# Optimization experiments

Hardware: AMD Instinct MI355X
Metric: run time of the kernel (lower is better)

## Reference

```python
import jax, jax.numpy as jnp
import numpy as np

N_HEADS = 12


def setup_inputs() -> dict:
    key = jax.random.key(0)
    ks = jax.random.split(key, 4)
    B, S, D = 2, 2048, 768
    x = jax.random.normal(ks[0], (B, S, D), dtype=jnp.float32)
    # nn.Linear-style init scale ~ 1/sqrt(D) to keep logits reasonable
    scale = 1.0 / np.sqrt(D)
    Wq = jax.random.normal(ks[1], (D, D), dtype=jnp.float32) * scale
    Wk = jax.random.normal(ks[2], (D, D), dtype=jnp.float32) * scale
    Wv = jax.random.normal(ks[3], (D, D), dtype=jnp.float32) * scale
    bq = jnp.zeros((D,), jnp.float32)
    bk = jnp.zeros((D,), jnp.float32)
    bv = jnp.zeros((D,), jnp.float32)
    mask = jnp.ones((B, S), jnp.int32)
    return {"x": x, "Wq": Wq, "bq": bq, "Wk": Wk, "bk": bk,
            "Wv": Wv, "bv": bv, "mask": mask}


def reference(x, Wq, bq, Wk, bk, Wv, bv, mask):
    B, S, D = x.shape
    H = N_HEADS
    W = D // H
    # q,k,v: (B,S,D) -> (B,H,S,W)
    def proj(Wm, bm):
        return (x @ Wm.T + bm).reshape(B, S, H, W).transpose(0, 2, 1, 3)
    q, k, v = proj(Wq, bq), proj(Wk, bk), proj(Wv, bv)
    scores = jnp.einsum("bhsw,bhtw->bhst", q, k) / jnp.sqrt(
        jnp.asarray(W, x.dtype))
    # mask: (B,S) -> broadcast over query positions; 0 -> -1e20
    scores = jnp.where(mask[:, None, None, :] == 0,
                       jnp.asarray(-1e20, scores.dtype), scores)
    attn = jax.nn.softmax(scores, axis=-1)  # (B,H,S,S)
    # dropout p=0.0 (eval) -> identity
    ctx = jnp.einsum("bhst,bhtw->bhsw", attn, v)
    hidden = ctx.transpose(0, 2, 1, 3).reshape(B, S, D)
    return hidden
```

## Files before the change

### kernel.cpp

```cpp
#include <hip/hip_runtime.h>
#include <hip/hip_bf16.h>
#include <stdint.h>


typedef __attribute__((ext_vector_type(8))) short bf16x8;
typedef __attribute__((ext_vector_type(4))) float f32x4;
typedef __attribute__((ext_vector_type(16))) float f32x16;
typedef __attribute__((ext_vector_type(8))) unsigned short u16x8;

#define MFMA16(a, b, c) __builtin_amdgcn_mfma_f32_16x16x32_bf16((a), (b), (c), 0, 0, 0)
#define MFMA32(a, b, c) __builtin_amdgcn_mfma_f32_32x32x16_bf16((a), (b), (c), 0, 0, 0)
#define SWZ(row, colb) ((colb) ^ (((row) & 7) << 4))

union U32x4BF {
  unsigned u[4];
  bf16x8 v;
};

__device__ __forceinline__ void gl_lds16(const void* g, void* l) {
  __builtin_amdgcn_global_load_lds(
      (__attribute__((address_space(1))) void*)const_cast<void*>(g),
      (__attribute__((address_space(3))) void*)l, 16, 0, 0);
}

__device__ __forceinline__ unsigned short f2bf(float x) {
  unsigned int v = __float_as_uint(x);
  return (unsigned short)((v + 0x7fffu + ((v >> 16) & 1u)) >> 16);
}

__global__ __launch_bounds__(256) void cvt_all(
    const float* __restrict__ x, const float* __restrict__ wq,
    const float* __restrict__ wk, const float* __restrict__ wv,
    unsigned short* __restrict__ xb, unsigned short* __restrict__ wb) {
  int i = blockIdx.x * 256 + threadIdx.x;
  const float* s;
  unsigned short* d;
  int off;
  if (i < 393216)      { s = x;  d = xb;            off = i; }
  else if (i < 466944) { s = wq; d = wb;            off = i - 393216; }
  else if (i < 540672) { s = wk; d = wb + 589824;   off = i - 466944; }
  else                 { s = wv; d = wb + 1179648;  off = i - 540672; }
  const float4* sp = (const float4*)s + (size_t)off * 2;
  float4 a = sp[0], b2 = sp[1];
  u16x8 o;
  o[0] = f2bf(a.x); o[1] = f2bf(a.y); o[2] = f2bf(a.z); o[3] = f2bf(a.w);
  o[4] = f2bf(b2.x); o[5] = f2bf(b2.y); o[6] = f2bf(b2.z); o[7] = f2bf(b2.w);
  *((u16x8*)d + off) = o;
}

__global__ __launch_bounds__(256) void proj_gemm(
    const unsigned short* __restrict__ xb, const unsigned short* __restrict__ wb,
    const float* __restrict__ bq, const float* __restrict__ bk, const float* __restrict__ bv,
    unsigned short* __restrict__ qw, unsigned short* __restrict__ kw,
    unsigned short* __restrict__ vw) {
  __shared__ __align__(16) char psmem[36864];
  const int t = threadIdx.x, lane = t & 63, w = t >> 6;
  const int lo = lane & 15, hi = lane >> 4;
  const int mbase = blockIdx.x * 64;
  const int wsel = blockIdx.y / 6;
  const int nbase = (blockIdx.y % 6) * 128;
  const char* xc = (const char*)xb;
  const char* wmc = (const char*)(wb + (size_t)wsel * 589824);

  const int tA = t * 16;
  const int arA = tA >> 7, acA = (tA & 127) ^ ((arA & 7) << 4);
  const int mA = ((acA >> 6) << 5) + arA, kA = acA & 63;
  const int pB0 = t * 16, pB1 = t * 16 + 4096;
  const int rB0 = pB0 >> 7, cB0 = (pB0 & 127) ^ ((rB0 & 7) << 4);
  const int nB0 = ((cB0 >> 6) << 6) + rB0, kB0 = cB0 & 63;
  const int rB1 = pB1 >> 7, cB1 = (pB1 & 127) ^ ((rB1 & 7) << 4);
  const int nB1 = ((cB1 >> 6) << 6) + rB1, kB1 = cB1 & 63;

  const char* xa0 = xc + (size_t)(mbase + mA) * 1536 + kA;
  const char* wa0 = wmc + (size_t)(nbase + nB0) * 1536 + kB0;
  const char* wa1 = wmc + (size_t)(nbase + nB1) * 1536 + kB1;

#define PSTAGE(BUF)                              \
  do {                                           \
    char* lb = psmem + (BUF) * 12288;            \
    gl_lds16(xa0, lb + tA);                      \
    gl_lds16(wa0, lb + 4096 + pB0);              \
    gl_lds16(wa1, lb + 4096 + pB1);              \
    xa0 += 64; wa0 += 64; wa1 += 64;             \
  } while (0)

  f32x4 acc[4][2];
#pragma unroll
  for (int i = 0; i < 4; i++)
#pragma unroll
    for (int j = 0; j < 2; j++) acc[i][j] = (f32x4){0.f, 0.f, 0.f, 0.f};

  PSTAGE(0);
  PSTAGE(1);
  int cur = 0, sb = 2;
#pragma unroll 1
  for (int it = 0; it < 24; ++it) {
    if (it < 22) {
      PSTAGE(sb);
      asm volatile("s_waitcnt vmcnt(6)" ::: "memory");
    } else if (it == 22) {
      asm volatile("s_waitcnt vmcnt(3)" ::: "memory");
    } else {
      asm volatile("s_waitcnt vmcnt(0)" ::: "memory");
    }
    __builtin_amdgcn_s_barrier();
    const char* lA = psmem + cur * 12288;
    const char* lB = lA + 4096;

    bf16x8 af[4], bf[2];
#pragma unroll
    for (int mf = 0; mf < 4; mf++) {
      int row = mf * 16 + lo;
      af[mf] = *(const bf16x8*)(lA + (row & 31) * 128 +
                                ((((row >> 5) << 6) + hi * 16) ^ ((row & 7) << 4)));
    }
#pragma unroll
    for (int nf = 0; nf < 2; nf++) {
      int n = w * 32 + nf * 16 + lo;
      bf[nf] = *(const bf16x8*)(lB + (n & 63) * 128 +
                                ((((n >> 6) << 6) + hi * 16) ^ ((n & 7) << 4)));
    }

    __builtin_amdgcn_s_setprio(1);
    if (wsel == 2) {
#pragma unroll
      for (int mf = 0; mf < 4; mf++)
#pragma unroll
        for (int nf = 0; nf < 2; nf++) acc[mf][nf] = MFMA16(bf[nf], af[mf], acc[mf][nf]);
    } else {
#pragma unroll
      for (int mf = 0; mf < 4; mf++)
#pragma unroll
        for (int nf = 0; nf < 2; nf++) acc[mf][nf] = MFMA16(af[mf], bf[nf], acc[mf][nf]);
    }
    __builtin_amdgcn_s_setprio(0);
    __builtin_amdgcn_s_barrier();
    cur = (cur == 2) ? 0 : cur + 1;
    sb = (sb == 2) ? 0 : sb + 1;
  }
#undef PSTAGE

  const float QSCALE = 0.125f * 1.44269504089f;
  if (wsel == 2) {
#pragma unroll
    for (int nf = 0; nf < 2; nf++) {
#pragma unroll
      for (int mf = 0; mf < 4; mf++) {
#pragma unroll
        for (int r = 0; r < 4; r++) {
          int n = nbase + w * 32 + nf * 16 + hi * 4 + r;
          int m = mbase + mf * 16 + lo;
          int b_ = m >> 11, s = m & 2047;
          int h = n >> 6, wcol = n & 63;
          float val = acc[mf][nf][r] + bv[n];
          vw[(((size_t)b_ * 12 + h) * 64 + wcol) * 2048 + s] = f2bf(val);
        }
      }
    }
  } else {
    const float* bias = (wsel == 0) ? bq : bk;
#pragma unroll
    for (int nf = 0; nf < 2; nf++) {
      int n = nbase + w * 32 + nf * 16 + lo;
      float bv_ = bias[n];
      int h = n >> 6, wcol = n & 63;
#pragma unroll
      for (int mf = 0; mf < 4; mf++) {
#pragma unroll
        for (int r = 0; r < 4; r++) {
          int m = mbase + mf * 16 + hi * 4 + r;
          int b_ = m >> 11, s = m & 2047;
          float val = acc[mf][nf][r] + bv_;
          size_t bhh = (size_t)b_ * 12 + h;
          if (wsel == 0)
            qw[(bhh * 2048 + s) * 64 + wcol] = f2bf(val * QSCALE);
          else
            kw[(bhh * 2048 + s) * 64 + wcol] = f2bf(val);
        }
      }
    }
  }
}

__global__ __launch_bounds__(256) void relayout_kv(
    const unsigned short* kw, const unsigned short* __restrict__ vwT,
    unsigned short* __restrict__ kx, unsigned short* vx) {
  __shared__ __align__(16) char rsm[32768];
  const int t = threadIdx.x;
  const int bid = blockIdx.x;
  const int xcd = bid & 7, sidx = bid >> 3;
  const int bh = xcd + 8 * (sidx % 3);
  const int ktq = sidx / 3;
  const size_t bhb = (size_t)bh * 262144;
  const int kt0 = ktq * 4;

  {
    const int key = t >> 3;
    const int d0 = (t & 7) * 8;
    const char* ksrc = (const char*)kw + bhb + (size_t)kt0 * 4096 + key * 128 + d0 * 2;
    char* kldst = rsm + (d0 >> 4) * 1024 + ((d0 >> 3) & 1) * 512 + key * 16;
#pragma unroll
    for (int c = 0; c < 4; c++)
      *(u16x8*)(kldst + c * 4096) = *(const u16x8*)(ksrc + c * 4096);
  }
  {
    const int w = t >> 2;
    const int sl0 = (t & 3) * 8;
    const char* vsrc = (const char*)vwT + bhb + (size_t)w * 4096 + (kt0 * 32 + sl0) * 2;
    char* vldst = rsm + 16384 + (w >> 5) * 2048 + ((sl0 >> 4) & 1) * 1024 +
                  ((sl0 >> 3) & 1) * 512 + (w & 31) * 16;
#pragma unroll
    for (int c = 0; c < 4; c++)
      *(u16x8*)(vldst + c * 4096) = *(const u16x8*)(vsrc + c * 64);
  }
  __syncthreads();

  char* kdst = (char*)kx + bhb + (size_t)ktq * 16384;
  char* vdst = (char*)vx + bhb + (size_t)ktq * 16384;
#pragma unroll
  for (int c = 0; c < 4; c++) {
    int lb = c * 4096 + t * 16;
    *(u16x8*)(kdst + lb) = *(const u16x8*)(rsm + lb);
    *(u16x8*)(vdst + lb) = *(const u16x8*)(rsm + 16384 + lb);
  }
}

__global__ __launch_bounds__(256) void attn_kernel(
    const unsigned short* __restrict__ qw, const unsigned short* __restrict__ kx,
    const unsigned short* __restrict__ vx, const int* __restrict__ mask,
    float* __restrict__ out) {
  __shared__ __align__(16) char smem[17152];
  const int t = threadIdx.x, lane = t & 63, wave = t >> 6;
  const int wq = wave >> 1, wk = wave & 1;
  const int l31 = lane & 31, hl = lane >> 5;
  const int bid = blockIdx.x;
  const int xcd = bid & 7, sidx = bid >> 3;
  const int bh = xcd + 8 * (sidx % 3);
  const int qb = sidx / 3;
  const int b = bh / 12, hh = bh - b * 12;

  {
    const int* mb = mask + (size_t)b * 2048 + t * 8;
    int4 a0 = *(const int4*)mb;
    int4 a1 = *(const int4*)(mb + 4);
    unsigned by = (unsigned)(a0.x != 0) | ((unsigned)(a0.y != 0) << 1) |
                  ((unsigned)(a0.z != 0) << 2) | ((unsigned)(a0.w != 0) << 3) |
                  ((unsigned)(a1.x != 0) << 4) | ((unsigned)(a1.y != 0) << 5) |
                  ((unsigned)(a1.z != 0) << 6) | ((unsigned)(a1.w != 0) << 7);
    smem[16384 + t] = (char)by;
  }
  __syncthreads();
  const unsigned balv = *(const unsigned*)(smem + 16384 + (wk * 32 + l31) * 4);

  bf16x8 qv[4];
  {
    int qrow = qb * 64 + wq * 32 + l31;
    const char* qp = (const char*)qw + ((size_t)bh * 2048 + qrow) * 128 + hl * 16;
#pragma unroll
    for (int s = 0; s < 4; s++) qv[s] = *(const bf16x8*)(qp + s * 32);
  }

  const char* kp = (const char*)kx + (size_t)bh * 262144 + (size_t)wk * 131072 + lane * 16;
  const char* vp = (const char*)vx + (size_t)bh * 262144 + (size_t)wk * 131072 + lane * 16;

  f32x16 oacc[2];
#pragma unroll
  for (int wh = 0; wh < 2; wh++)
#pragma unroll
    for (int g = 0; g < 16; g++) oacc[wh][g] = 0.f;
  float lacc = 0.f;

  bf16x8 ka0 = *(const bf16x8*)(kp);
  bf16x8 ka1 = *(const bf16x8*)(kp + 1024);
  bf16x8 ka2 = *(const bf16x8*)(kp + 2048);
  bf16x8 ka3 = *(const bf16x8*)(kp + 3072);
  kp += 4096;

#pragma unroll 2
  for (int it = 0; it < 32; ++it) {
    bf16x8 v00 = *(const bf16x8*)(vp);
    bf16x8 v01 = *(const bf16x8*)(vp + 1024);
    bf16x8 v10 = *(const bf16x8*)(vp + 2048);
    bf16x8 v11 = *(const bf16x8*)(vp + 3072);
    vp += 4096;

    f32x16 sc;
#pragma unroll
    for (int g = 0; g < 16; g++) sc[g] = 0.f;
    __builtin_amdgcn_s_setprio(1);
    sc = MFMA32(ka0, qv[0], sc);
    sc = MFMA32(ka1, qv[1], sc);
    sc = MFMA32(ka2, qv[2], sc);
    sc = MFMA32(ka3, qv[3], sc);
    __builtin_amdgcn_s_setprio(0);

    ka0 = *(const bf16x8*)(kp);
    ka1 = *(const bf16x8*)(kp + 1024);
    ka2 = *(const bf16x8*)(kp + 2048);
    ka3 = *(const bf16x8*)(kp + 3072);
    kp += 4096;

    unsigned bal = __builtin_amdgcn_readlane(balv, it);
    if (bal != 0xFFFFFFFFu) {
#pragma unroll
      for (int g = 0; g < 16; g++) {
        int key = (g & 3) + 8 * (g >> 2) + 4 * hl;
        if (!((bal >> key) & 1)) sc[g] = -30000.f;
      }
    }

#pragma unroll
    for (int g = 0; g < 16; g++) {
      float e_;
      asm("v_exp_f32 %0, %1" : "=v"(e_) : "v"(sc[g]));
      sc[g] = e_;
    }
    unsigned pk[4][2];
#pragma unroll
    for (int m = 0; m < 4; m++) {
      asm("v_cvt_pk_bf16_f32 %0, %1, %2" : "=v"(pk[m][0]) : "v"(sc[4 * m]), "v"(sc[4 * m + 1]));
      asm("v_cvt_pk_bf16_f32 %0, %1, %2" : "=v"(pk[m][1]) : "v"(sc[4 * m + 2]), "v"(sc[4 * m + 3]));
    }
    U32x4BF apv[2];
#pragma unroll
    for (int sp = 0; sp < 2; sp++)
#pragma unroll
      for (int cp = 0; cp < 2; cp++) {
        unsigned xx = pk[2 * sp][cp], yy = pk[2 * sp + 1][cp];
        asm("v_permlane32_swap_b32 %0, %1" : "+v"(xx), "+v"(yy));
        apv[sp].u[cp] = xx;
        apv[sp].u[2 + cp] = yy;
      }

    __builtin_amdgcn_s_setprio(1);
    oacc[0] = MFMA32(apv[0].v, v00, oacc[0]);
    oacc[0] = MFMA32(apv[1].v, v01, oacc[0]);
    oacc[1] = MFMA32(apv[0].v, v10, oacc[1]);
    oacc[1] = MFMA32(apv[1].v, v11, oacc[1]);
    __builtin_amdgcn_s_setprio(0);

    lacc += (((sc[0] + sc[1]) + (sc[2] + sc[3])) + ((sc[4] + sc[5]) + (sc[6] + sc[7]))) +
            (((sc[8] + sc[9]) + (sc[10] + sc[11])) + ((sc[12] + sc[13]) + (sc[14] + sc[15])));
  }

  lacc += __shfl_xor(lacc, 32);
  if (lane < 32)
    *(float*)(smem + 16640 + (((wq * 32 + l31) << 1) + wk) * 4) = lacc;
  if (wk == 1) {
#pragma unroll
    for (int wh = 0; wh < 2; wh++) {
      int vrow = wh * 32 + l31;
#pragma unroll
      for (int m = 0; m < 4; m++) {
        f32x4 part = (f32x4){oacc[wh][4 * m], oacc[wh][4 * m + 1],
                             oacc[wh][4 * m + 2], oacc[wh][4 * m + 3]};
        *(f32x4*)(smem + wq * 8192 + vrow * 128 + SWZ(vrow, hl * 16 + m * 32)) = part;
      }
    }
  }
  __syncthreads();
  if (wk == 0) {
    float linv[16];
#pragma unroll
    for (int g = 0; g < 16; g++) {
      int qrow = 4 * hl + (g & 3) + 8 * (g >> 2);
      float2 lp = *(const float2*)(smem + 16640 + ((wq * 32 + qrow) << 3));
      linv[g] = __builtin_amdgcn_rcpf(lp.x + lp.y);
    }
#pragma unroll
    for (int wh = 0; wh < 2; wh++) {
      int vrow = wh * 32 + l31;
#pragma unroll
      for (int m = 0; m < 4; m++) {
        f32x4 part = *(const f32x4*)(smem + wq * 8192 + vrow * 128 + SWZ(vrow, hl * 16 + m * 32));
#pragma unroll
        for (int r = 0; r < 4; r++) {
          int g = 4 * m + r;
          int qrow = 4 * hl + r + 8 * m;
          float val = (oacc[wh][g] + part[r]) * linv[g];
          out[((size_t)b * 2048 + qb * 64 + wq * 32 + qrow) * 768 + hh * 64 + wh * 32 + l31] =
              val;
        }
      }
    }
  }
}

extern "C" void kernel_launch(void* const* d_in, const int* in_sizes, int n_in,
                              void* d_out, int out_size, void* d_ws, size_t ws_size,
                              hipStream_t stream) {
  (void)in_sizes; (void)n_in; (void)out_size; (void)ws_size;
  const float* x  = (const float*)d_in[0];
  const float* Wq = (const float*)d_in[1];
  const float* bq = (const float*)d_in[2];
  const float* Wk = (const float*)d_in[3];
  const float* bk = (const float*)d_in[4];
  const float* Wv = (const float*)d_in[5];
  const float* bv = (const float*)d_in[6];
  const int* mask = (const int*)d_in[7];
  float* out = (float*)d_out;

  char* ws = (char*)d_ws;
  unsigned short* xb  = (unsigned short*)(ws);
  unsigned short* wb  = (unsigned short*)(ws + 6291456);
  unsigned short* qw  = (unsigned short*)(ws + 9830400);
  unsigned short* kw  = (unsigned short*)(ws + 16121856);
  unsigned short* vwT = (unsigned short*)(ws + 22413312);
  unsigned short* kx  = (unsigned short*)(ws);
  unsigned short* vx  = (unsigned short*)(ws + 16121856);

  cvt_all<<<2400, 256, 0, stream>>>(x, Wq, Wk, Wv, xb, wb);
  proj_gemm<<<dim3(64, 18), 256, 0, stream>>>(xb, wb, bq, bk, bv, qw, kw, vwT);
  relayout_kv<<<384, 256, 0, stream>>>(kw, vwT, kx, vx);
  attn_kernel<<<768, 256, 0, stream>>>(qw, kx, vx, mask, out);
}
```

Before: 83.21 us.

## Software-pipeline QK^T MFMA one tile ahead of softmax and PV

Restructures the attention inner loop so the score MFMAs for tile i are issued while tile i-1's mask, exp, bf16 packing and PV MFMAs are processed, ping-ponging between two score accumulators. This is meant to hide MFMA latency and keep the matrix units busy during the VALU exp/convert work. It costs an extra 16-float accumulator in registers, which may lower occupancy, and adds a prologue and epilogue.

```diff
diff --git a/kernel.cpp b/kernel.cpp
--- a/kernel.cpp
+++ b/kernel.cpp
@@ -263,85 +263,110 @@
   const char* kp = (const char*)kx + (size_t)bh * 262144 + (size_t)wk * 131072 + lane * 16;
   const char* vp = (const char*)vx + (size_t)bh * 262144 + (size_t)wk * 131072 + lane * 16;
 
-  f32x16 oacc[2];
+  f32x16 oacc[2], scA, scB;
 #pragma unroll
   for (int wh = 0; wh < 2; wh++)
 #pragma unroll
     for (int g = 0; g < 16; g++) oacc[wh][g] = 0.f;
   float lacc = 0.f;
-
-  bf16x8 ka0 = *(const bf16x8*)(kp);
-  bf16x8 ka1 = *(const bf16x8*)(kp + 1024);
-  bf16x8 ka2 = *(const bf16x8*)(kp + 2048);
-  bf16x8 ka3 = *(const bf16x8*)(kp + 3072);
+  bf16x8 v00, v01, v10, v11;
+  bf16x8 ka0, ka1, ka2, ka3;
+
+#define SMPV(J_, SCP_)                                                                   \
+  {                                                                                      \
+    unsigned bal_ = __builtin_amdgcn_readlane(balv, (J_));                               \
+    if (bal_ != 0xFFFFFFFFu) {                                                           \
+      _Pragma("unroll") for (int g = 0; g < 16; g++) {                                   \
+        int key_ = (g & 3) + 8 * (g >> 2) + 4 * hl;                                      \
+        if (!((bal_ >> key_) & 1)) SCP_[g] = -30000.f;                                   \
+      }                                                                                  \
+    }                                                                                    \
+    _Pragma("unroll") for (int g = 0; g < 16; g++) {                                     \
+      float e_;                                                                          \
+      asm("v_exp_f32 %0, %1" : "=v"(e_) : "v"(SCP_[g]));                                 \
+      SCP_[g] = e_;                                                                      \
+    }                                                                                    \
+    unsigned pk_[4][2];                                                                  \
+    _Pragma("unroll") for (int m = 0; m < 4; m++) {                                      \
+      asm("v_cvt_pk_bf16_f32 %0, %1, %2"                                                 \
+          : "=v"(pk_[m][0]) : "v"(SCP_[4 * m]), "v"(SCP_[4 * m + 1]));                   \
+      asm("v_cvt_pk_bf16_f32 %0, %1, %2"                                                 \
+          : "=v"(pk_[m][1]) : "v"(SCP_[4 * m + 2]), "v"(SCP_[4 * m + 3]));               \
+    }                                                                                    \
+    U32x4BF apv_[2];                                                                     \
+    _Pragma("unroll") for (int sp = 0; sp < 2; sp++)                                     \
+        _Pragma("unroll") for (int cp = 0; cp < 2; cp++) {                               \
+      unsigned xx_ = pk_[2 * sp][cp], yy_ = pk_[2 * sp + 1][cp];                         \
+      asm("v_permlane32_swap_b32 %0, %1" : "+v"(xx_), "+v"(yy_));                        \
+      apv_[sp].u[cp] = xx_;                                                              \
+      apv_[sp].u[2 + cp] = yy_;                                                          \
+    }                                                                                    \
+    __builtin_amdgcn_s_setprio(1);                                                       \
+    oacc[0] = MFMA32(apv_[0].v, v00, oacc[0]);                                           \
+    oacc[0] = MFMA32(apv_[1].v, v01, oacc[0]);                                           \
+    oacc[1] = MFMA32(apv_[0].v, v10, oacc[1]);                                           \
+    oacc[1] = MFMA32(apv_[1].v, v11, oacc[1]);                                           \
+    __builtin_amdgcn_s_setprio(0);                                                       \
+    lacc += (((SCP_[0] + SCP_[1]) + (SCP_[2] + SCP_[3])) +                               \
+             ((SCP_[4] + SCP_[5]) + (SCP_[6] + SCP_[7]))) +                              \
+            (((SCP_[8] + SCP_[9]) + (SCP_[10] + SCP_[11])) +                             \
+             ((SCP_[12] + SCP_[13]) + (SCP_[14] + SCP_[15])));                           \
+  }
+
+#define BODY(IT_, SCQ_, SCP_)                                                            \
+  {                                                                                      \
+    v00 = *(const bf16x8*)(vp);                                                          \
+    v01 = *(const bf16x8*)(vp + 1024);                                                   \
+    v10 = *(const bf16x8*)(vp + 2048);                                                   \
+    v11 = *(const bf16x8*)(vp + 3072);                                                   \
+    vp += 4096;                                                                          \
+    _Pragma("unroll") for (int g = 0; g < 16; g++) SCQ_[g] = 0.f;                        \
+    __builtin_amdgcn_s_setprio(1);                                                       \
+    SCQ_ = MFMA32(ka0, qv[0], SCQ_);                                                     \
+    SCQ_ = MFMA32(ka1, qv[1], SCQ_);                                                     \
+    SCQ_ = MFMA32(ka2, qv[2], SCQ_);                                                     \
+    SCQ_ = MFMA32(ka3, qv[3], SCQ_);                                                     \
+    __builtin_amdgcn_s_setprio(0);                                                       \
+    ka0 = *(const bf16x8*)(kp);                                                          \
+    ka1 = *(const bf16x8*)(kp + 1024);                                                   \
+    ka2 = *(const bf16x8*)(kp + 2048);                                                   \
+    ka3 = *(const bf16x8*)(kp + 3072);                                                   \
+    kp += 4096;                                                                          \
+    SMPV((IT_) - 1, SCP_);                                                               \
+  }
+
+  ka0 = *(const bf16x8*)(kp);
+  ka1 = *(const bf16x8*)(kp + 1024);
+  ka2 = *(const bf16x8*)(kp + 2048);
+  ka3 = *(const bf16x8*)(kp + 3072);
   kp += 4096;
-
-#pragma unroll 2
-  for (int it = 0; it < 32; ++it) {
-    bf16x8 v00 = *(const bf16x8*)(vp);
-    bf16x8 v01 = *(const bf16x8*)(vp + 1024);
-    bf16x8 v10 = *(const bf16x8*)(vp + 2048);
-    bf16x8 v11 = *(const bf16x8*)(vp + 3072);
-    vp += 4096;
-
-    f32x16 sc;
-#pragma unroll
-    for (int g = 0; g < 16; g++) sc[g] = 0.f;
-    __builtin_amdgcn_s_setprio(1);
-    sc = MFMA32(ka0, qv[0], sc);
-    sc = MFMA32(ka1, qv[1], sc);
-    sc = MFMA32(ka2, qv[2], sc);
-    sc = MFMA32(ka3, qv[3], sc);
-    __builtin_amdgcn_s_setprio(0);
-
-    ka0 = *(const bf16x8*)(kp);
-    ka1 = *(const bf16x8*)(kp + 1024);
-    ka2 = *(const bf16x8*)(kp + 2048);
-    ka3 = *(const bf16x8*)(kp + 3072);
-    kp += 4096;
-
-    unsigned bal = __builtin_amdgcn_readlane(balv, it);
-    if (bal != 0xFFFFFFFFu) {
-#pragma unroll
-      for (int g = 0; g < 16; g++) {
-        int key = (g & 3) + 8 * (g >> 2) + 4 * hl;
-        if (!((bal >> key) & 1)) sc[g] = -30000.f;
-      }
-    }
-
-#pragma unroll
-    for (int g = 0; g < 16; g++) {
-      float e_;
-      asm("v_exp_f32 %0, %1" : "=v"(e_) : "v"(sc[g]));
-      sc[g] = e_;
-    }
-    unsigned pk[4][2];
-#pragma unroll
-    for (int m = 0; m < 4; m++) {
-      asm("v_cvt_pk_bf16_f32 %0, %1, %2" : "=v"(pk[m][0]) : "v"(sc[4 * m]), "v"(sc[4 * m + 1]));
-      asm("v_cvt_pk_bf16_f32 %0, %1, %2" : "=v"(pk[m][1]) : "v"(sc[4 * m + 2]), "v"(sc[4 * m + 3]));
-    }
-    U32x4BF apv[2];
-#pragma unroll
-    for (int sp = 0; sp < 2; sp++)
-#pragma unroll
-      for (int cp = 0; cp < 2; cp++) {
-        unsigned xx = pk[2 * sp][cp], yy = pk[2 * sp + 1][cp];
-        asm("v_permlane32_swap_b32 %0, %1" : "+v"(xx), "+v"(yy));
-        apv[sp].u[cp] = xx;
-        apv[sp].u[2 + cp] = yy;
-      }
-
-    __builtin_amdgcn_s_setprio(1);
-    oacc[0] = MFMA32(apv[0].v, v00, oacc[0]);
-    oacc[0] = MFMA32(apv[1].v, v01, oacc[0]);
-    oacc[1] = MFMA32(apv[0].v, v10, oacc[1]);
-    oacc[1] = MFMA32(apv[1].v, v11, oacc[1]);
-    __builtin_amdgcn_s_setprio(0);
-
-    lacc += (((sc[0] + sc[1]) + (sc[2] + sc[3])) + ((sc[4] + sc[5]) + (sc[6] + sc[7]))) +
-            (((sc[8] + sc[9]) + (sc[10] + sc[11])) + ((sc[12] + sc[13]) + (sc[14] + sc[15])));
-  }
+#pragma unroll
+  for (int g = 0; g < 16; g++) scA[g] = 0.f;
+  scA = MFMA32(ka0, qv[0], scA);
+  scA = MFMA32(ka1, qv[1], scA);
+  scA = MFMA32(ka2, qv[2], scA);
+  scA = MFMA32(ka3, qv[3], scA);
+  ka0 = *(const bf16x8*)(kp);
+  ka1 = *(const bf16x8*)(kp + 1024);
+  ka2 = *(const bf16x8*)(kp + 2048);
+  ka3 = *(const bf16x8*)(kp + 3072);
+  kp += 4096;
+
+#pragma unroll 1
+  for (int itb = 1; itb < 31; itb += 2) {
+    BODY(itb, scB, scA);
+    BODY(itb + 1, scA, scB);
+  }
+  BODY(31, scB, scA);
+  {
+    v00 = *(const bf16x8*)(vp);
+    v01 = *(const bf16x8*)(vp + 1024);
+    v10 = *(const bf16x8*)(vp + 2048);
+    v11 = *(const bf16x8*)(vp + 3072);
+    SMPV(31, scB);
+  }
+#undef BODY
+#undef SMPV
 
   lacc += __shfl_xor(lacc, 32);
   if (lane < 32)
```

New measurement: 82.54 us. Within noise of the previous version (-0.8%).
